# Optimization experiments

Measured on AMD Instinct MI355X. Metric: run time of the kernel, lower is better.

Reference implementation:

```python
import jax, jax.numpy as jnp
import numpy as np

N = 50000   # nodes
E = 600000  # edges (time_feat is per-edge: same mask indexes k and src_idx)
D = 128     # adapter_dim
C = 8       # num_clusters
SCALE = D ** -0.5


def setup_inputs() -> dict:
    key = jax.random.key(0)
    ks = jax.random.split(key, 12)
    s = 1.0 / np.sqrt(D)
    return {
        "node_feat": jax.random.normal(ks[0], (N, D), jnp.float32),
        "time_feat": jax.random.normal(ks[1], (E, D), jnp.float32),
        "context_feat": jax.random.normal(ks[2], (N, D), jnp.float32),
        "edge_index": jax.random.randint(ks[3], (2, E), 0, N),
        "Wq": jax.random.uniform(ks[4], (D, D), jnp.float32, -s, s),
        "bq": jnp.zeros((D,), jnp.float32),
        "Wk": jax.random.uniform(ks[5], (D, D), jnp.float32, -s, s),
        "bk": jnp.zeros((D,), jnp.float32),
        "Wv": jax.random.uniform(ks[6], (D, D), jnp.float32, -s, s),
        "bv": jnp.zeros((D,), jnp.float32),
        "cluster_emb": jax.random.normal(ks[7], (C, D), jnp.float32),
        "Wo": jax.random.uniform(ks[8], (D, D), jnp.float32, -s, s),
        "bo": jnp.zeros((D,), jnp.float32),
    }


def reference(node_feat, time_feat, context_feat, edge_index,
              Wq, bq, Wk, bk, Wv, bv, cluster_emb, Wo, bo):
    q = node_feat @ Wq + bq            # [N, D]
    k = time_feat @ Wk + bk            # [E, D]
    v = time_feat @ Wv + bv            # [E, D]

    # cluster routing: argmax(softmax(sim)) == argmax(sim)
    sim = (time_feat @ cluster_emb.T) * SCALE   # [E, C]
    assign = jnp.argmax(sim, axis=-1)           # [E] int

    src = edge_index[0]                          # [E]
    seg = assign * N + src                       # combined (cluster, dst-of-scatter) segment id
    nseg = C * N

    attn = jnp.sum(q[src] * k, axis=-1) * SCALE  # [E]

    # scatter_softmax per (cluster, src node)
    seg_max = jax.ops.segment_max(attn, seg, num_segments=nseg)
    ex = jnp.exp(attn - seg_max[seg])
    denom = jax.ops.segment_sum(ex, seg, num_segments=nseg)
    w = ex / denom[seg]                          # [E]

    # scatter_mean per (cluster, src node) -> [C, N, D]
    wv = v * w[:, None]
    sums = jax.ops.segment_sum(wv, seg, num_segments=nseg)                 # [C*N, D]
    counts = jax.ops.segment_sum(jnp.ones((E,), v.dtype), seg, num_segments=nseg)
    means = sums / jnp.maximum(counts, 1.0)[:, None]                       # empty -> 0
    per_cluster = means.reshape(C, N, D)

    # sum(outputs) / len(outputs): only non-empty clusters contribute an entry
    edges_per_cluster = jax.ops.segment_sum(jnp.ones((E,), jnp.float32), assign, num_segments=C)
    num_nonempty = jnp.sum((edges_per_cluster > 0).astype(jnp.float32))
    combined = per_cluster.sum(axis=0) / num_nonempty                      # [N, D]

    return jax.nn.relu(combined @ Wo + bo)
```

## Files before the change

### kernel.cpp

```cpp
#include <hip/hip_runtime.h>
#include <math.h>


#define NN 50000
#define NE 600000
#define DD 128
#define NC 8
#define CAP 48
#define SCALEF 0.08838834764831845f

#define OFF_NODECNT  0
#define OFF_FILL     50000
#define OFF_MASK     100000
#define ZERO_ELEMS   100256
#define OFF_NODEOFF  100352
#define OFF_PARTIAL  150352
#define OFF_BQK      150608
#define OFF_BVO      150736
#define OFF_WQBK     150864
#define OFF_C0       150992
#define OFF_WQK      151008
#define OFF_WVO      167392
#define OFF_QB       183776
#define OFF_SORTED   233776
#define OFF_SW       833776
#define OFF_EXV      883776
#define OFF_ASSIGN   1483776
#define OFF_P        2083776

__global__ __launch_bounds__(256) void k_pre_count(
    const float* __restrict__ Wq, const float* __restrict__ bq,
    const float* __restrict__ Wk, const float* __restrict__ bk,
    const float* __restrict__ Wv, const float* __restrict__ bv,
    const float* __restrict__ Wo, const int* __restrict__ ei,
    int* __restrict__ node_cnt,
    float* __restrict__ Wqk, float* __restrict__ bqk,
    float* __restrict__ Wvo, float* __restrict__ bvo,
    float* __restrict__ wqbk, float* __restrict__ c0) {
  int bid = blockIdx.x, t = threadIdx.x;
  if (bid >= 129) {
    long e = (long)(bid - 129) * 256 + t;
    if (e < NE) atomicAdd(&node_cnt[ei[e]], 1);
    return;
  }
  __shared__ float rq[DD], rv[DD];
  int b = bid;
  if (b < DD) {
    if (t < DD) { rq[t] = Wq[b * DD + t]; rv[t] = Wv[b * DD + t]; }
    __syncthreads();
    if (t < DD) {
      float aq = 0.f, av = 0.f;
      for (int j = 0; j < DD; j++) {
        aq += rq[j] * Wk[t * DD + j];
        av += rv[j] * Wo[j * DD + t];
      }
      Wqk[b * DD + t] = aq;
      Wvo[b * DD + t] = av;
    }
  } else {
    if (t < DD) {
      float a1 = 0.f, a2 = 0.f, a3 = 0.f;
      for (int j = 0; j < DD; j++) {
        a1 += bq[j] * Wk[t * DD + j];
        a2 += bv[j] * Wo[j * DD + t];
        a3 += Wq[t * DD + j] * bk[j];
      }
      bqk[t] = a1; bvo[t] = a2; wqbk[t] = a3;
      if (t == 0) {
        float s = 0.f;
        for (int j = 0; j < DD; j++) s += bq[j] * bk[j];
        *c0 = s;
      }
    }
  }
}

__global__ __launch_bounds__(256) void k_p(
    const float* __restrict__ nf, const float* __restrict__ Wqk,
    const float* __restrict__ bqk, const float* __restrict__ wqbk,
    const float* __restrict__ c0p,
    float* __restrict__ p, float* __restrict__ qb) {
  __shared__ float a_lds[64 * DD];
  __shared__ float wb_lds[DD];
  int t = threadIdx.x;
  long row0 = (long)blockIdx.x * 64;
  for (int it = 0; it < 8; it++) {
    int idx = (it * 256 + t) * 4;
    long r = row0 + idx / DD;
    float4 v = {0.f, 0.f, 0.f, 0.f};
    if (r < NN) v = *(const float4*)(nf + r * DD + (idx % DD));
    *(float4*)(a_lds + idx) = v;
  }
  if (t < DD) wb_lds[t] = wqbk[t];
  __syncthreads();
  int cg = t % 32, rg = t / 32;
  int col0 = cg * 4, r0 = rg * 8;
  float acc[8][4]; float qacc[8];
  for (int r = 0; r < 8; r++) { qacc[r] = 0.f; for (int c = 0; c < 4; c++) acc[r][c] = 0.f; }
  for (int k = 0; k < DD; k++) {
    float4 b4 = *(const float4*)(Wqk + k * DD + col0);
    float wbk = wb_lds[k];
    for (int r = 0; r < 8; r++) {
      float a = a_lds[(r0 + r) * DD + k];
      acc[r][0] += a * b4.x; acc[r][1] += a * b4.y;
      acc[r][2] += a * b4.z; acc[r][3] += a * b4.w;
      qacc[r] += a * wbk;
    }
  }
  float4 bq4 = *(const float4*)(bqk + col0);
  float c0v = *c0p;
  for (int r = 0; r < 8; r++) {
    long row = row0 + r0 + r;
    if (row < NN) {
      float4 o;
      o.x = acc[r][0] + bq4.x; o.y = acc[r][1] + bq4.y;
      o.z = acc[r][2] + bq4.z; o.w = acc[r][3] + bq4.w;
      *(float4*)(p + row * DD + col0) = o;
      if (cg == 0) qb[row] = qacc[r] + c0v;
    }
  }
}

__global__ __launch_bounds__(256) void k_scan1(const int* __restrict__ node_cnt,
                                               int* __restrict__ partial) {
  int i = blockIdx.x * 256 + threadIdx.x;
  int v = (i < NN) ? node_cnt[i] : 0;
  for (int o = 1; o < 64; o <<= 1) v += __shfl_xor(v, o);
  __shared__ int wsum[4];
  if ((threadIdx.x & 63) == 0) wsum[threadIdx.x >> 6] = v;
  __syncthreads();
  if (threadIdx.x == 0) partial[blockIdx.x] = wsum[0] + wsum[1] + wsum[2] + wsum[3];
}

__global__ __launch_bounds__(256) void k_scan2(int* __restrict__ partial) {
  __shared__ int s[256];
  int t = threadIdx.x;
  int v = (t < 196) ? partial[t] : 0;
  s[t] = v;
  __syncthreads();
  for (int o = 1; o < 256; o <<= 1) {
    int add = (t >= o) ? s[t - o] : 0;
    __syncthreads();
    s[t] += add;
    __syncthreads();
  }
  if (t < 196) partial[t] = s[t] - v;
}

__global__ __launch_bounds__(256) void k_scan3(const int* __restrict__ node_cnt,
                                               const int* __restrict__ partial,
                                               int* __restrict__ node_off) {
  __shared__ int s[256];
  int t = threadIdx.x;
  int i = blockIdx.x * 256 + t;
  int v = (i < NN) ? node_cnt[i] : 0;
  s[t] = v;
  __syncthreads();
  for (int o = 1; o < 256; o <<= 1) {
    int add = (t >= o) ? s[t - o] : 0;
    __syncthreads();
    s[t] += add;
    __syncthreads();
  }
  if (i < NN) node_off[i] = partial[blockIdx.x] + s[t] - v;
}

__global__ __launch_bounds__(256) void k_scatter(const int* __restrict__ ei,
                                                 const int* __restrict__ node_off,
                                                 int* __restrict__ fill,
                                                 int* __restrict__ sorted) {
  long e = (long)blockIdx.x * 256 + threadIdx.x;
  if (e < NE) {
    int s = ei[e];
    int pos = node_off[s] + atomicAdd(&fill[s], 1);
    sorted[pos] = (int)e;
  }
}

__device__ __forceinline__ void sim_attn_edge(
    const float* t_lds, const float* ce_lds, const float* p_lds, float qbv,
    int el, int j, float& ex_out, int& bc_out) {
  const float* trow = t_lds + el * DD;
  int sw8 = el & 7;
  float4 tv[8];
  for (int i = 0; i < 8; i++)
    tv[i] = *(const float4*)(trow + ((i * 4 + j) ^ sw8) * 4);
  float sims[NC];
  for (int c = 0; c < NC; c++) {
    const float* cr = ce_lds + c * DD;
    float s = 0.f;
    for (int i = 0; i < 8; i++) {
      float4 cv = *(const float4*)(cr + (i * 4 + j) * 4);
      s += tv[i].x * cv.x + tv[i].y * cv.y + tv[i].z * cv.z + tv[i].w * cv.w;
    }
    sims[c] = s;
  }
  float a = 0.f;
  for (int i = 0; i < 8; i++) {
    float4 pv = *(const float4*)(p_lds + (i * 4 + j) * 4);
    a += tv[i].x * pv.x + tv[i].y * pv.y + tv[i].z * pv.z + tv[i].w * pv.w;
  }
  for (int c = 0; c < NC; c++) {
    sims[c] += __shfl_xor(sims[c], 1);
    sims[c] += __shfl_xor(sims[c], 2);
  }
  a += __shfl_xor(a, 1);
  a += __shfl_xor(a, 2);
  float best = sims[0]; int bc = 0;
  for (int c = 1; c < NC; c++) if (sims[c] > best) { best = sims[c]; bc = c; }
  ex_out = expf((a + qbv) * SCALEF);
  bc_out = bc;
}

__global__ __launch_bounds__(256) void k_fused(
    const float* __restrict__ tf, const int* __restrict__ sorted,
    const int* __restrict__ node_off, const int* __restrict__ node_cnt,
    const float* __restrict__ ce, const float* __restrict__ p,
    const float* __restrict__ qb,
    float* __restrict__ exv_g, int* __restrict__ assign_g,
    int* __restrict__ maskArr,
    float* __restrict__ agg, float* __restrict__ sw) {
  __shared__ float t_lds[CAP * DD];
  __shared__ float ce_lds[NC * DD];
  __shared__ float p_lds[DD];
  __shared__ float team_lds[DD];
  __shared__ float exf[CAP];
  __shared__ float scl[CAP];
  __shared__ int   cli[CAP];
  __shared__ int   eidx[CAP];
  __shared__ float D_sh[NC];
  __shared__ int   C_sh[NC];
  __shared__ float qb_sh;

  int n = blockIdx.x;
  int t = threadIdx.x;
  int off = node_off[n], cnt = node_cnt[n];

  if (cnt == 0) {
    if (t < 32) {
      float4 z = {0.f, 0.f, 0.f, 0.f};
      *(float4*)(agg + (long)n * DD + t * 4) = z;
    }
    if (t == 0) sw[n] = 0.f;
    return;
  }

  *(float4*)(ce_lds + t * 4) = *(const float4*)(ce + t * 4);
  if (t < 32) *(float4*)(p_lds + t * 4) = *(const float4*)(p + (long)n * DD + t * 4);
  if (t < NC) { D_sh[t] = 0.f; C_sh[t] = 0; }
  if (t == 0) qb_sh = qb[n];

  int el = t >> 2, j = t & 3;
  int d = t & 127, team = t >> 7;
  float aggacc = 0.f;

  if (cnt <= CAP) {
    if (t < cnt) eidx[t] = sorted[off + t];
    __syncthreads();
    int total4 = cnt * 32;
    for (int i = t; i < total4; i += 256) {
      int e_i = i >> 5, d4 = i & 31;
      *(float4*)(t_lds + e_i * DD + (d4 ^ (e_i & 7)) * 4) =
          *(const float4*)(tf + (long)eidx[e_i] * DD + d4 * 4);
    }
    __syncthreads();
    if (el < cnt) {
      float ex; int bc;
      sim_attn_edge(t_lds, ce_lds, p_lds, qb_sh, el, j, ex, bc);
      if (j == 0) {
        exf[el] = ex; cli[el] = bc;
        atomicAdd(&D_sh[bc], ex);
        atomicAdd(&C_sh[bc], 1);
      }
    }
    __syncthreads();
    if (t < cnt) scl[t] = exf[t] / (D_sh[cli[t]] * (float)C_sh[cli[t]]);
    if (t == 0) {
      int m = 0; float s = 0.f;
      for (int c = 0; c < NC; c++)
        if (C_sh[c] > 0) { m |= 1 << c; s += 1.0f / (float)C_sh[c]; }
      atomicOr(&maskArr[n & 255], m);
      sw[n] = s;
    }
    __syncthreads();
    for (int e = team; e < cnt; e += 2)
      aggacc += scl[e] * t_lds[e * DD + (((d >> 2) ^ (e & 7)) << 2) + (d & 3)];
  } else {
    int nchunk = (cnt + CAP - 1) / CAP;
    for (int ch = 0; ch < nchunk; ch++) {
      int base = ch * CAP;
      int m = cnt - base; if (m > CAP) m = CAP;
      __syncthreads();
      if (t < m) eidx[t] = sorted[off + base + t];
      __syncthreads();
      int total4 = m * 32;
      for (int i = t; i < total4; i += 256) {
        int e_i = i >> 5, d4 = i & 31;
        *(float4*)(t_lds + e_i * DD + (d4 ^ (e_i & 7)) * 4) =
            *(const float4*)(tf + (long)eidx[e_i] * DD + d4 * 4);
      }
      __syncthreads();
      if (el < m) {
        float ex; int bc;
        sim_attn_edge(t_lds, ce_lds, p_lds, qb_sh, el, j, ex, bc);
        if (j == 0) {
          exv_g[off + base + el] = ex;
          assign_g[off + base + el] = bc;
          atomicAdd(&D_sh[bc], ex);
          atomicAdd(&C_sh[bc], 1);
        }
      }
    }
    __syncthreads();
    if (t == 0) {
      int m = 0; float s = 0.f;
      for (int c = 0; c < NC; c++)
        if (C_sh[c] > 0) { m |= 1 << c; s += 1.0f / (float)C_sh[c]; }
      atomicOr(&maskArr[n & 255], m);
      sw[n] = s;
    }
    for (int ch = 0; ch < nchunk; ch++) {
      int base = ch * CAP;
      int m = cnt - base; if (m > CAP) m = CAP;
      __syncthreads();
      if (t < m) {
        eidx[t] = sorted[off + base + t];
        int c = assign_g[off + base + t];
        scl[t] = exv_g[off + base + t] / (D_sh[c] * (float)C_sh[c]);
      }
      __syncthreads();
      int total4 = m * 32;
      for (int i = t; i < total4; i += 256) {
        int e_i = i >> 5, d4 = i & 31;
        *(float4*)(t_lds + e_i * DD + (d4 ^ (e_i & 7)) * 4) =
            *(const float4*)(tf + (long)eidx[e_i] * DD + d4 * 4);
      }
      __syncthreads();
      for (int e = team; e < m; e += 2)
        aggacc += scl[e] * t_lds[e * DD + (((d >> 2) ^ (e & 7)) << 2) + (d & 3)];
    }
  }
  if (team == 1) team_lds[d] = aggacc;
  __syncthreads();
  if (team == 0) agg[(long)n * DD + d] = aggacc + team_lds[d];
}

__global__ __launch_bounds__(256) void k_out(
    const float* __restrict__ agg, const float* __restrict__ Wvo,
    const float* __restrict__ bvo, const float* __restrict__ sw,
    const float* __restrict__ bo, const int* __restrict__ maskArr,
    float* __restrict__ out) {
  __shared__ float a_lds[64 * DD];
  __shared__ float sw_lds[64];
  __shared__ int morw[4];
  int t = threadIdx.x;
  int mv = maskArr[t];
  for (int o = 1; o < 64; o <<= 1) mv |= __shfl_xor(mv, o);
  if ((t & 63) == 0) morw[t >> 6] = mv;
  long row0 = (long)blockIdx.x * 64;
  for (int it = 0; it < 8; it++) {
    int idx = (it * 256 + t) * 4;
    long r = row0 + idx / DD;
    float4 v = {0.f, 0.f, 0.f, 0.f};
    if (r < NN) v = *(const float4*)(agg + r * DD + (idx % DD));
    *(float4*)(a_lds + idx) = v;
  }
  if (t < 64) {
    long r = row0 + t;
    sw_lds[t] = (r < NN) ? sw[r] : 0.f;
  }
  __syncthreads();
  int full = morw[0] | morw[1] | morw[2] | morw[3];
  int nne = __popc(full); if (nne == 0) nne = 1;
  float inv = 1.0f / (float)nne;
  int cg = t % 32, rg = t / 32;
  int col0 = cg * 4, r0 = rg * 8;
  float acc[8][4];
  for (int r = 0; r < 8; r++) for (int c = 0; c < 4; c++) acc[r][c] = 0.f;
  for (int k = 0; k < DD; k++) {
    float4 b4 = *(const float4*)(Wvo + k * DD + col0);
    for (int r = 0; r < 8; r++) {
      float a = a_lds[(r0 + r) * DD + k];
      acc[r][0] += a * b4.x; acc[r][1] += a * b4.y;
      acc[r][2] += a * b4.z; acc[r][3] += a * b4.w;
    }
  }
  float4 bv4 = *(const float4*)(bvo + col0);
  float4 bo4 = *(const float4*)(bo + col0);
  for (int r = 0; r < 8; r++) {
    long row = row0 + r0 + r;
    if (row < NN) {
      float s = sw_lds[r0 + r];
      float4 o;
      o.x = fmaxf((acc[r][0] + s * bv4.x) * inv + bo4.x, 0.f);
      o.y = fmaxf((acc[r][1] + s * bv4.y) * inv + bo4.y, 0.f);
      o.z = fmaxf((acc[r][2] + s * bv4.z) * inv + bo4.z, 0.f);
      o.w = fmaxf((acc[r][3] + s * bv4.w) * inv + bo4.w, 0.f);
      *(float4*)(out + row * DD + col0) = o;
    }
  }
}

extern "C" void kernel_launch(void* const* d_in, const int* in_sizes, int n_in,
                              void* d_out, int out_size, void* d_ws, size_t ws_size,
                              hipStream_t stream) {
  const float* nf = (const float*)d_in[0];
  const float* tf = (const float*)d_in[1];
  const int*   ei = (const int*)d_in[3];
  const float* Wq = (const float*)d_in[4];
  const float* bq = (const float*)d_in[5];
  const float* Wk = (const float*)d_in[6];
  const float* bk = (const float*)d_in[7];
  const float* Wv = (const float*)d_in[8];
  const float* bv = (const float*)d_in[9];
  const float* ce = (const float*)d_in[10];
  const float* Wo = (const float*)d_in[11];
  const float* bo = (const float*)d_in[12];
  float* out = (float*)d_out;

  float* ws  = (float*)d_ws;
  int*   node_cnt = (int*)(ws + OFF_NODECNT);
  int*   fill     = (int*)(ws + OFF_FILL);
  int*   maskArr  = (int*)(ws + OFF_MASK);
  int*   node_off = (int*)(ws + OFF_NODEOFF);
  int*   partial  = (int*)(ws + OFF_PARTIAL);
  float* bqk      = ws + OFF_BQK;
  float* bvo      = ws + OFF_BVO;
  float* wqbk     = ws + OFF_WQBK;
  float* c0       = ws + OFF_C0;
  float* Wqk      = ws + OFF_WQK;
  float* Wvo      = ws + OFF_WVO;
  float* qb       = ws + OFF_QB;
  int*   sorted   = (int*)(ws + OFF_SORTED);
  float* sw       = ws + OFF_SW;
  float* exv      = ws + OFF_EXV;
  int*   assign   = (int*)(ws + OFF_ASSIGN);
  float* p        = ws + OFF_P;
  float* agg      = ws + OFF_P;

  hipMemsetAsync(d_ws, 0, (size_t)ZERO_ELEMS * 4, stream);

  k_pre_count<<<129 + (NE + 255) / 256, 256, 0, stream>>>(
      Wq, bq, Wk, bk, Wv, bv, Wo, ei, node_cnt, Wqk, bqk, Wvo, bvo, wqbk, c0);
  k_p<<<(NN + 63) / 64, 256, 0, stream>>>(nf, Wqk, bqk, wqbk, c0, p, qb);
  k_scan1<<<196, 256, 0, stream>>>(node_cnt, partial);
  k_scan2<<<1, 256, 0, stream>>>(partial);
  k_scan3<<<196, 256, 0, stream>>>(node_cnt, partial, node_off);
  k_scatter<<<(NE + 255) / 256, 256, 0, stream>>>(ei, node_off, fill, sorted);
  k_fused<<<NN, 256, 0, stream>>>(tf, sorted, node_off, node_cnt, ce, p, qb,
                                  exv, assign, maskArr, agg, sw);
  k_out<<<(NN + 63) / 64, 256, 0, stream>>>(agg, Wvo, bvo, sw, bo, maskArr, out);
}
```

Baseline: 805.0 us.

## Process edge windows per block instead of one block per node

Replaces the one-block-per-node fused kernel with blocks that each own a window of about 64 sorted edges, located by binary search over node offsets in the scatter kernel. Each block computes attention and cluster assignment for 32-edge chunks, then accumulates per-cluster weighted sums in LDS and flushes a node whenever the source changes. This is meant to cut the cost of 50000 mostly tiny blocks and the two-pass global spill for high-degree nodes. The price is serial per-edge accumulation loops with branchy flushes and more LDS state per block.

```diff
diff --git a/kernel.cpp b/kernel.cpp
--- a/kernel.cpp
+++ b/kernel.cpp
@@ -6,7 +6,11 @@
 #define NE 600000
 #define DD 128
 #define NC 8
-#define CAP 48
+#define WIN 64
+#define NWIN 9376
+#define NBF  9377
+#define CHK 32
+#define NLOC 64
 #define SCALEF 0.08838834764831845f
 
 #define OFF_NODECNT  0
@@ -15,18 +19,18 @@
 #define ZERO_ELEMS   100256
 #define OFF_NODEOFF  100352
 #define OFF_PARTIAL  150352
-#define OFF_BQK      150608
-#define OFF_BVO      150736
-#define OFF_WQBK     150864
-#define OFF_C0       150992
-#define OFF_WQK      151008
-#define OFF_WVO      167392
-#define OFF_QB       183776
-#define OFF_SORTED   233776
-#define OFF_SW       833776
-#define OFF_EXV      883776
-#define OFF_ASSIGN   1483776
-#define OFF_P        2083776
+#define OFF_BF       150608
+#define OFF_BQK      160000
+#define OFF_BVO      160128
+#define OFF_WQBK     160256
+#define OFF_C0       160384
+#define OFF_WQK      160400
+#define OFF_WVO      176784
+#define OFF_QB       193168
+#define OFF_SORTED   243168
+#define OFF_SRCS     843168
+#define OFF_SW       1443168
+#define OFF_P        1493168
 
 __global__ __launch_bounds__(256) void k_pre_count(
     const float* __restrict__ Wq, const float* __restrict__ bq,
@@ -165,184 +169,178 @@
   if (i < NN) node_off[i] = partial[blockIdx.x] + s[t] - v;
 }
 
+#define EDGE_BLKS 2344
+#define BS_BLKS   37
 __global__ __launch_bounds__(256) void k_scatter(const int* __restrict__ ei,
                                                  const int* __restrict__ node_off,
                                                  int* __restrict__ fill,
-                                                 int* __restrict__ sorted) {
-  long e = (long)blockIdx.x * 256 + threadIdx.x;
+                                                 int* __restrict__ sorted,
+                                                 int* __restrict__ srcs,
+                                                 int* __restrict__ blockFirst) {
+  int bid = blockIdx.x, t = threadIdx.x;
+  if (bid >= EDGE_BLKS) {
+    int w = (bid - EDGE_BLKS) * 256 + t;
+    if (w < NBF) {
+      int v = w * WIN, lo = 0, hi = NN;
+      while (lo < hi) { int mid = (lo + hi) >> 1; if (node_off[mid] < v) lo = mid + 1; else hi = mid; }
+      blockFirst[w] = lo;
+    }
+    return;
+  }
+  long e = (long)bid * 256 + t;
   if (e < NE) {
     int s = ei[e];
     int pos = node_off[s] + atomicAdd(&fill[s], 1);
     sorted[pos] = (int)e;
-  }
-}
-
-__device__ __forceinline__ void sim_attn_edge(
-    const float* t_lds, const float* ce_lds, const float* p_lds, float qbv,
-    int el, int j, float& ex_out, int& bc_out) {
-  const float* trow = t_lds + el * DD;
-  int sw8 = el & 7;
-  float4 tv[8];
-  for (int i = 0; i < 8; i++)
-    tv[i] = *(const float4*)(trow + ((i * 4 + j) ^ sw8) * 4);
-  float sims[NC];
-  for (int c = 0; c < NC; c++) {
-    const float* cr = ce_lds + c * DD;
-    float s = 0.f;
-    for (int i = 0; i < 8; i++) {
-      float4 cv = *(const float4*)(cr + (i * 4 + j) * 4);
-      s += tv[i].x * cv.x + tv[i].y * cv.y + tv[i].z * cv.z + tv[i].w * cv.w;
-    }
-    sims[c] = s;
-  }
-  float a = 0.f;
-  for (int i = 0; i < 8; i++) {
-    float4 pv = *(const float4*)(p_lds + (i * 4 + j) * 4);
-    a += tv[i].x * pv.x + tv[i].y * pv.y + tv[i].z * pv.z + tv[i].w * pv.w;
-  }
-  for (int c = 0; c < NC; c++) {
-    sims[c] += __shfl_xor(sims[c], 1);
-    sims[c] += __shfl_xor(sims[c], 2);
-  }
-  a += __shfl_xor(a, 1);
-  a += __shfl_xor(a, 2);
-  float best = sims[0]; int bc = 0;
-  for (int c = 1; c < NC; c++) if (sims[c] > best) { best = sims[c]; bc = c; }
-  ex_out = expf((a + qbv) * SCALEF);
-  bc_out = bc;
-}
-
-__global__ __launch_bounds__(256) void k_fused(
+    srcs[pos] = s;
+  }
+}
+
+__global__ __launch_bounds__(256) void k_fused2(
     const float* __restrict__ tf, const int* __restrict__ sorted,
-    const int* __restrict__ node_off, const int* __restrict__ node_cnt,
+    const int* __restrict__ srcs, const int* __restrict__ node_off,
+    const int* __restrict__ node_cnt, const int* __restrict__ blockFirst,
     const float* __restrict__ ce, const float* __restrict__ p,
-    const float* __restrict__ qb,
-    float* __restrict__ exv_g, int* __restrict__ assign_g,
-    int* __restrict__ maskArr,
+    const float* __restrict__ qb, int* __restrict__ maskArr,
     float* __restrict__ agg, float* __restrict__ sw) {
-  __shared__ float t_lds[CAP * DD];
   __shared__ float ce_lds[NC * DD];
-  __shared__ float p_lds[DD];
-  __shared__ float team_lds[DD];
-  __shared__ float exf[CAP];
-  __shared__ float scl[CAP];
-  __shared__ int   cli[CAP];
-  __shared__ int   eidx[CAP];
-  __shared__ float D_sh[NC];
-  __shared__ int   C_sh[NC];
-  __shared__ float qb_sh;
-
-  int n = blockIdx.x;
-  int t = threadIdx.x;
-  int off = node_off[n], cnt = node_cnt[n];
-
-  if (cnt == 0) {
-    if (t < 32) {
-      float4 z = {0.f, 0.f, 0.f, 0.f};
-      *(float4*)(agg + (long)n * DD + t * 4) = z;
-    }
-    if (t == 0) sw[n] = 0.f;
-    return;
-  }
+  __shared__ float t_lds[CHK * DD];
+  __shared__ float U_sh[NC * DD];
+  __shared__ float D_sh[NLOC * NC];
+  __shared__ int   C_sh[NLOC * NC];
+  __shared__ float exf_sh[CHK];
+  __shared__ int   cli_sh[CHK];
+  __shared__ int   eidx_sh[CHK];
+  __shared__ int   srcs_sh[CHK];
+  __shared__ int   cnt0_sh[NLOC];
+
+  int t = threadIdx.x, b = blockIdx.x;
+  int fn = blockFirst[b], ln = blockFirst[b + 1] - 1;
+  if (fn >= NN || ln < fn) return;
 
   *(float4*)(ce_lds + t * 4) = *(const float4*)(ce + t * 4);
-  if (t < 32) *(float4*)(p_lds + t * 4) = *(const float4*)(p + (long)n * DD + t * 4);
-  if (t < NC) { D_sh[t] = 0.f; C_sh[t] = 0; }
-  if (t == 0) qb_sh = qb[n];
-
-  int el = t >> 2, j = t & 3;
-  int d = t & 127, team = t >> 7;
-  float aggacc = 0.f;
-
-  if (cnt <= CAP) {
-    if (t < cnt) eidx[t] = sorted[off + t];
-    __syncthreads();
-    int total4 = cnt * 32;
-    for (int i = t; i < total4; i += 256) {
-      int e_i = i >> 5, d4 = i & 31;
-      *(float4*)(t_lds + e_i * DD + (d4 ^ (e_i & 7)) * 4) =
-          *(const float4*)(tf + (long)eidx[e_i] * DD + d4 * 4);
-    }
-    __syncthreads();
-    if (el < cnt) {
-      float ex; int bc;
-      sim_attn_edge(t_lds, ce_lds, p_lds, qb_sh, el, j, ex, bc);
-      if (j == 0) {
-        exf[el] = ex; cli[el] = bc;
-        atomicAdd(&D_sh[bc], ex);
-        atomicAdd(&C_sh[bc], 1);
-      }
-    }
-    __syncthreads();
-    if (t < cnt) scl[t] = exf[t] / (D_sh[cli[t]] * (float)C_sh[cli[t]]);
-    if (t == 0) {
-      int m = 0; float s = 0.f;
-      for (int c = 0; c < NC; c++)
-        if (C_sh[c] > 0) { m |= 1 << c; s += 1.0f / (float)C_sh[c]; }
-      atomicOr(&maskArr[n & 255], m);
-      sw[n] = s;
-    }
-    __syncthreads();
-    for (int e = team; e < cnt; e += 2)
-      aggacc += scl[e] * t_lds[e * DD + (((d >> 2) ^ (e & 7)) << 2) + (d & 3)];
-  } else {
-    int nchunk = (cnt + CAP - 1) / CAP;
-    for (int ch = 0; ch < nchunk; ch++) {
-      int base = ch * CAP;
-      int m = cnt - base; if (m > CAP) m = CAP;
+
+  int el = t >> 3, j = t & 7;
+  int d = t & 127;
+  int msk_acc = 0;
+
+  for (int s0 = fn; s0 <= ln; s0 += NLOC) {
+    int e2 = s0 + NLOC - 1; if (e2 > ln) e2 = ln;
+    int nN = e2 - s0 + 1;
+    int eb = node_off[s0];
+    int ee = node_off[e2] + node_cnt[e2];
+    for (int i = t; i < NLOC * NC; i += 256) { D_sh[i] = 0.f; C_sh[i] = 0; }
+    for (int i = t; i < NC * DD; i += 256) U_sh[i] = 0.f;
+    if (t < nN) cnt0_sh[t] = node_cnt[s0 + t];
+    __syncthreads();
+
+    for (int n = 0; n < nN; n++) {
+      if (cnt0_sh[n] == 0) {
+        if (t < DD) agg[(long)(s0 + n) * DD + t] = 0.f;
+        if (t == 0) sw[s0 + n] = 0.f;
+      }
+    }
+
+    int cur = -1;
+    auto do_flush = [&](int node) {
+      int l = (node - s0) * NC;
+      if (t < DD) {
+        float acc = 0.f;
+        #pragma unroll
+        for (int c = 0; c < NC; c++) {
+          int cc = C_sh[l + c];
+          if (cc > 0)
+            acc += U_sh[c * DD + d] * __builtin_amdgcn_rcpf(D_sh[l + c] * (float)cc);
+          U_sh[c * DD + d] = 0.f;
+        }
+        agg[(long)node * DD + d] = acc;
+      }
+      if (t == 0) {
+        float ssw = 0.f; int mk = 0;
+        #pragma unroll
+        for (int c = 0; c < NC; c++) {
+          int cc = C_sh[l + c];
+          if (cc > 0) { mk |= 1 << c; ssw += __builtin_amdgcn_rcpf((float)cc); }
+        }
+        sw[node] = ssw; msk_acc |= mk;
+      }
+    };
+
+    for (int c0 = eb; c0 < ee; c0 += CHK) {
+      int m = ee - c0; if (m > CHK) m = CHK;
+      if (t < m) { eidx_sh[t] = sorted[c0 + t]; srcs_sh[t] = srcs[c0 + t]; }
       __syncthreads();
-      if (t < m) eidx[t] = sorted[off + base + t];
+
+      if (el < m) {
+        long eid = eidx_sh[el];
+        int src = srcs_sh[el];
+        const float* trow = tf + eid * DD;
+        const float* prow = p + (long)src * DD;
+        float4 tv[4];
+        #pragma unroll
+        for (int i = 0; i < 4; i++) tv[i] = *(const float4*)(trow + (i * 8 + j) * 4);
+        int sw8 = el & 7;
+        #pragma unroll
+        for (int i = 0; i < 4; i++)
+          *(float4*)(t_lds + el * DD + (((i * 8 + j) ^ sw8) << 2)) = tv[i];
+        float a = 0.f;
+        #pragma unroll
+        for (int i = 0; i < 4; i++) {
+          float4 pv = *(const float4*)(prow + (i * 8 + j) * 4);
+          a += tv[i].x * pv.x + tv[i].y * pv.y + tv[i].z * pv.z + tv[i].w * pv.w;
+        }
+        float sims[NC];
+        #pragma unroll
+        for (int c = 0; c < NC; c++) {
+          const float* cr = ce_lds + c * DD;
+          float sacc = 0.f;
+          #pragma unroll
+          for (int i = 0; i < 4; i++) {
+            float4 cv = *(const float4*)(cr + (i * 8 + j) * 4);
+            sacc += tv[i].x * cv.x + tv[i].y * cv.y + tv[i].z * cv.z + tv[i].w * cv.w;
+          }
+          sims[c] = sacc;
+        }
+        #pragma unroll
+        for (int c = 0; c < NC; c++) {
+          sims[c] += __shfl_xor(sims[c], 1);
+          sims[c] += __shfl_xor(sims[c], 2);
+          sims[c] += __shfl_xor(sims[c], 4);
+        }
+        a += __shfl_xor(a, 1);
+        a += __shfl_xor(a, 2);
+        a += __shfl_xor(a, 4);
+        if (j == 0) {
+          float best = sims[0]; int bc = 0;
+          #pragma unroll
+          for (int c = 1; c < NC; c++) if (sims[c] > best) { best = sims[c]; bc = c; }
+          float ex = expf((a + qb[src]) * SCALEF);
+          exf_sh[el] = ex; cli_sh[el] = bc;
+          int l = (src - s0) * NC + bc;
+          atomicAdd(&D_sh[l], ex);
+          atomicAdd(&C_sh[l], 1);
+        }
+      }
       __syncthreads();
-      int total4 = m * 32;
-      for (int i = t; i < total4; i += 256) {
-        int e_i = i >> 5, d4 = i & 31;
-        *(float4*)(t_lds + e_i * DD + (d4 ^ (e_i & 7)) * 4) =
-            *(const float4*)(tf + (long)eidx[e_i] * DD + d4 * 4);
+
+      for (int ii = 0; ii < m; ii++) {
+        int sv = srcs_sh[ii];
+        if (sv != cur) {
+          if (cur >= 0) do_flush(cur);
+          cur = sv;
+        }
+        if (t < DD) {
+          int c = cli_sh[ii];
+          float tval = t_lds[ii * DD + ((((d >> 2) ^ (ii & 7)) << 2) | (d & 3))];
+          U_sh[c * DD + d] += exf_sh[ii] * tval;
+        }
       }
       __syncthreads();
-      if (el < m) {
-        float ex; int bc;
-        sim_attn_edge(t_lds, ce_lds, p_lds, qb_sh, el, j, ex, bc);
-        if (j == 0) {
-          exv_g[off + base + el] = ex;
-          assign_g[off + base + el] = bc;
-          atomicAdd(&D_sh[bc], ex);
-          atomicAdd(&C_sh[bc], 1);
-        }
-      }
-    }
-    __syncthreads();
-    if (t == 0) {
-      int m = 0; float s = 0.f;
-      for (int c = 0; c < NC; c++)
-        if (C_sh[c] > 0) { m |= 1 << c; s += 1.0f / (float)C_sh[c]; }
-      atomicOr(&maskArr[n & 255], m);
-      sw[n] = s;
-    }
-    for (int ch = 0; ch < nchunk; ch++) {
-      int base = ch * CAP;
-      int m = cnt - base; if (m > CAP) m = CAP;
-      __syncthreads();
-      if (t < m) {
-        eidx[t] = sorted[off + base + t];
-        int c = assign_g[off + base + t];
-        scl[t] = exv_g[off + base + t] / (D_sh[c] * (float)C_sh[c]);
-      }
-      __syncthreads();
-      int total4 = m * 32;
-      for (int i = t; i < total4; i += 256) {
-        int e_i = i >> 5, d4 = i & 31;
-        *(float4*)(t_lds + e_i * DD + (d4 ^ (e_i & 7)) * 4) =
-            *(const float4*)(tf + (long)eidx[e_i] * DD + d4 * 4);
-      }
-      __syncthreads();
-      for (int e = team; e < m; e += 2)
-        aggacc += scl[e] * t_lds[e * DD + (((d >> 2) ^ (e & 7)) << 2) + (d & 3)];
-    }
-  }
-  if (team == 1) team_lds[d] = aggacc;
-  __syncthreads();
-  if (team == 0) agg[(long)n * DD + d] = aggacc + team_lds[d];
+    }
+    if (cur >= 0) do_flush(cur);
+    __syncthreads();
+  }
+  if (t == 0 && msk_acc) atomicOr(&maskArr[b & 255], msk_acc);
 }
 
 __global__ __launch_bounds__(256) void k_out(
@@ -424,6 +422,7 @@
   int*   maskArr  = (int*)(ws + OFF_MASK);
   int*   node_off = (int*)(ws + OFF_NODEOFF);
   int*   partial  = (int*)(ws + OFF_PARTIAL);
+  int*   blockFirst = (int*)(ws + OFF_BF);
   float* bqk      = ws + OFF_BQK;
   float* bvo      = ws + OFF_BVO;
   float* wqbk     = ws + OFF_WQBK;
@@ -432,22 +431,22 @@
   float* Wvo      = ws + OFF_WVO;
   float* qb       = ws + OFF_QB;
   int*   sorted   = (int*)(ws + OFF_SORTED);
+  int*   srcs     = (int*)(ws + OFF_SRCS);
   float* sw       = ws + OFF_SW;
-  float* exv      = ws + OFF_EXV;
-  int*   assign   = (int*)(ws + OFF_ASSIGN);
   float* p        = ws + OFF_P;
   float* agg      = ws + OFF_P;
 
   hipMemsetAsync(d_ws, 0, (size_t)ZERO_ELEMS * 4, stream);
 
-  k_pre_count<<<129 + (NE + 255) / 256, 256, 0, stream>>>(
+  k_pre_count<<<129 + EDGE_BLKS, 256, 0, stream>>>(
       Wq, bq, Wk, bk, Wv, bv, Wo, ei, node_cnt, Wqk, bqk, Wvo, bvo, wqbk, c0);
   k_p<<<(NN + 63) / 64, 256, 0, stream>>>(nf, Wqk, bqk, wqbk, c0, p, qb);
   k_scan1<<<196, 256, 0, stream>>>(node_cnt, partial);
   k_scan2<<<1, 256, 0, stream>>>(partial);
   k_scan3<<<196, 256, 0, stream>>>(node_cnt, partial, node_off);
-  k_scatter<<<(NE + 255) / 256, 256, 0, stream>>>(ei, node_off, fill, sorted);
-  k_fused<<<NN, 256, 0, stream>>>(tf, sorted, node_off, node_cnt, ce, p, qb,
-                                  exv, assign, maskArr, agg, sw);
+  k_scatter<<<EDGE_BLKS + BS_BLKS, 256, 0, stream>>>(ei, node_off, fill, sorted,
+                                                     srcs, blockFirst);
+  k_fused2<<<NWIN, 256, 0, stream>>>(tf, sorted, srcs, node_off, node_cnt,
+                                     blockFirst, ce, p, qb, maskArr, agg, sw);
   k_out<<<(NN + 63) / 64, 256, 0, stream>>>(agg, Wvo, bvo, sw, bo, maskArr, out);
 }
```

New measurement: 745.1 us. -7.4%, faster.
